# Optimization experiments

Measured on AMD Instinct MI355X. Metric: run time of the kernel, lower is better.

## Reference

```python
import jax, jax.numpy as jnp
from jax import lax
import numpy as np

NUM_HEAD = 12
EPS = 1e-5            # torch LayerNorm default
NEG_INF = 1.0e12      # self.inf_value in the source
LEAKY_SLOPE = 0.01    # torch LeakyReLU default
MASK_FIRST = True     # maskedAtten=True applies only to block 0


def _layer_norm(x, s, b):
    m = jnp.mean(x, axis=-1, keepdims=True)
    v = jnp.var(x, axis=-1, keepdims=True)
    return (x - m) / jnp.sqrt(v + EPS) * s + b


def _forward(x, conv_w, conv_b, pos, ln0_s, ln0_b, Wq, bq, Wk, bk, Wv, bv,
             Wo, bo, ln1_s, ln1_b, W1, b1, W2, b2, proj_w, proj_b):
    B, C, H, W = x.shape
    E = conv_w.shape[0]
    P = conv_w.shape[-1]
    hd = E // NUM_HEAD

    # patch embed: Conv2d(C, E, P, stride=P)
    h = lax.conv_general_dilated(x, conv_w, (P, P), 'VALID',
                                 dimension_numbers=('NCHW', 'OIHW', 'NCHW'))
    h = h + conv_b[None, :, None, None]
    L = h.shape[2] * h.shape[3]
    h = h.reshape(B, E, L).transpose(0, 2, 1) + pos  # (B, L, E)

    causal = jnp.triu(jnp.ones((L, L), dtype=bool), 1)
    n_layers = Wq.shape[0]
    for i in range(n_layers):
        # --- attention block ---
        xn = _layer_norm(h, ln0_s[i], ln0_b[i])
        q = (xn @ Wq[i] + bq[i]).reshape(B, L, NUM_HEAD, hd).transpose(0, 2, 1, 3)
        k = (xn @ Wk[i] + bk[i]).reshape(B, L, NUM_HEAD, hd).transpose(0, 2, 1, 3)
        v = (xn @ Wv[i] + bv[i]).reshape(B, L, NUM_HEAD, hd).transpose(0, 2, 1, 3)
        scores = jnp.einsum('bhqd,bhkd->bhqk', q, k) * (hd ** -0.5)
        if i == 0 and MASK_FIRST:
            scores = jnp.where(causal, -NEG_INF, scores)
        a = jax.nn.softmax(scores, axis=-1)
        o = jnp.einsum('bhqk,bhkd->bhqd', a, v)  # (B, NH, L, hd)
        # faithful to torch source: reshape(bs, l, emb) WITHOUT permuting heads back
        o = o.reshape(B, L, E)
        o = o @ Wo[i] + bo[i]
        h = o + h  # residual onto pre-LN input
        # --- MLP block ---
        xr = _layer_norm(h, ln1_s[i], ln1_b[i])
        m = xr @ W1[i] + b1[i]
        m = jnp.where(m >= 0, m, LEAKY_SLOPE * m)
        m = m @ W2[i] + b2[i]
        h = m + xr  # residual onto post-LN (as in source)

    y = h @ proj_w + proj_b               # (B, L, C*P*P)
    y = y.transpose(0, 2, 1).reshape(B, C, H, W)
    return y


def setup_inputs() -> dict:
    key = jax.random.key(0)
    B, C, H, W = 8, 3, 384, 384
    P, E, NL = 16, 768, 8
    FF = 4 * E
    L = (H // P) * (W // P)  # 576
    CPP = C * P * P          # 768
    s = 0.02
    ks = jax.random.split(key, 24)
    f32 = jnp.float32
    inp = {
        'x': jax.random.normal(ks[0], (B, C, H, W), f32),
        'conv_w': jax.random.normal(ks[1], (E, C, P, P), f32) * s,
        'conv_b': jax.random.normal(ks[2], (E,), f32) * s,
        'pos': jax.random.normal(ks[3], (1, L, E), f32),
        'ln0_s': jnp.ones((NL, E), f32),
        'ln0_b': jnp.zeros((NL, E), f32),
        'Wq': jax.random.normal(ks[4], (NL, E, E), f32) * s,
        'bq': jax.random.normal(ks[5], (NL, E), f32) * s,
        'Wk': jax.random.normal(ks[6], (NL, E, E), f32) * s,
        'bk': jax.random.normal(ks[7], (NL, E), f32) * s,
        'Wv': jax.random.normal(ks[8], (NL, E, E), f32) * s,
        'bv': jax.random.normal(ks[9], (NL, E), f32) * s,
        'Wo': jax.random.normal(ks[10], (NL, E, E), f32) * s,
        'bo': jax.random.normal(ks[11], (NL, E), f32) * s,
        'ln1_s': jnp.ones((NL, E), f32),
        'ln1_b': jnp.zeros((NL, E), f32),
        'W1': jax.random.normal(ks[12], (NL, E, FF), f32) * s,
        'b1': jax.random.normal(ks[13], (NL, FF), f32) * s,
        'W2': jax.random.normal(ks[14], (NL, FF, E), f32) * s,
        'b2': jax.random.normal(ks[15], (NL, E), f32) * s,
        'proj_w': jax.random.normal(ks[16], (E, CPP), f32) * s,
        'proj_b': jax.random.normal(ks[17], (CPP,), f32) * s,
    }
    return inp


def reference(x, conv_w, conv_b, pos, ln0_s, ln0_b, Wq, bq, Wk, bk, Wv, bv,
              Wo, bo, ln1_s, ln1_b, W1, b1, W2, b2, proj_w, proj_b):
    return _forward(x, conv_w, conv_b, pos, ln0_s, ln0_b, Wq, bq, Wk, bk,
                    Wv, bv, Wo, bo, ln1_s, ln1_b, W1, b1, W2, b2,
                    proj_w, proj_b)
```

## Files before the change

kernel.cpp:

```cpp
#include <hip/hip_runtime.h>
#include <hip/hip_bf16.h>
#include <stdint.h>

#define NLAYERS 8
#define LSEQ 576
#define EMB 768
#define NHEAD 12
#define HDIM 64
#define FFDIM 3072
#define BLROWS 4608

typedef __attribute__((ext_vector_type(8))) short short8;
typedef __attribute__((ext_vector_type(4))) float floatx4;

__device__ __forceinline__ float b2f(short s) {
    union { float f; uint32_t u; } x; x.u = ((uint32_t)(uint16_t)s) << 16; return x.f;
}
__device__ __forceinline__ short f2b(float f) {
    union { float f; uint32_t u; } x; x.f = f;
    uint32_t r = x.u + 0x7fffu + ((x.u >> 16) & 1u);
    return (short)(r >> 16);
}

#define GLDS16(gp, lp) __builtin_amdgcn_global_load_lds( \
    (const __attribute__((address_space(1))) void*)(gp), \
    (__attribute__((address_space(3))) void*)(lp), 16, 0, 0)

__device__ __forceinline__ void xcd_remap(int& bx, int& by) {
    const int gx = gridDim.x;
    const int n  = gx * gridDim.y;
    const int orig = by * gx + bx;
    const int q = n >> 3, r = n & 7;
    const int xcd = orig & 7;
    const int wgid = (xcd < r ? xcd * (q + 1) : r * (q + 1) + (xcd - r) * q) + (orig >> 3);
    bx = wgid % gx;
    by = wgid / gx;
}

template<int DEPTH, int RES, bool ADD_POS, bool LEAKY, bool OUT_F32>
__global__ __launch_bounds__(256)
void gemm_bt(const short* __restrict__ A, const short* __restrict__ Bt,
             const float* __restrict__ bias, const float* __restrict__ pos,
             const void* __restrict__ res, void* __restrict__ Cout,
             int N, int K)
{
    __shared__ short As[DEPTH * 64 * 64];
    __shared__ short Bs[DEPTH * 128 * 64];
    int bx = blockIdx.x, by = blockIdx.y;
    xcd_remap(bx, by);
    const int t    = threadIdx.x;
    const int lane = t & 63;
    const int w    = t >> 6;
    const int m0   = by * 64;
    const int n0   = bx * 128;
    const int wm   = (w >> 1) * 32;
    const int wn   = (w & 1) * 64;

    floatx4 acc[2][4];
#pragma unroll
    for (int i = 0; i < 2; ++i)
#pragma unroll
        for (int j = 0; j < 4; ++j)
            acc[i][j] = (floatx4){0.f, 0.f, 0.f, 0.f};

    const int srow = t >> 3;
    const int sch  = t & 7;
    const short* Ag = A  + (size_t)m0 * K;
    const short* Bg = Bt + (size_t)n0 * K;
    const int nt = K >> 6;

#define STAGE(buf, k0)                                                              \
    {                                                                               \
        _Pragma("unroll")                                                           \
        for (int i = 0; i < 2; ++i) {                                               \
            int row = srow + i * 32;                                                \
            GLDS16(Ag + (size_t)row * K + (k0) + ((sch ^ (row & 7)) << 3),          \
                   &As[(buf) * 4096 + (size_t)(t + i * 256) * 8]);                  \
        }                                                                           \
        _Pragma("unroll")                                                           \
        for (int i = 0; i < 4; ++i) {                                               \
            int row = srow + i * 32;                                                \
            GLDS16(Bg + (size_t)row * K + (k0) + ((sch ^ (row & 7)) << 3),          \
                   &Bs[(buf) * 8192 + (size_t)(t + i * 256) * 8]);                  \
        }                                                                           \
    }

#define COMPUTE(buf)                                                                \
    {                                                                               \
        _Pragma("unroll")                                                           \
        for (int ks = 0; ks < 2; ++ks) {                                            \
            short8 af[2], bf[4];                                                    \
            _Pragma("unroll")                                                       \
            for (int i = 0; i < 2; ++i) {                                           \
                int row = wm + i * 16 + (lane & 15);                                \
                int ch  = (ks * 4 + (lane >> 4)) ^ (row & 7);                       \
                af[i] = *(const short8*)&As[(buf) * 4096 + row * 64 + ch * 8];      \
            }                                                                       \
            _Pragma("unroll")                                                       \
            for (int j = 0; j < 4; ++j) {                                           \
                int row = wn + j * 16 + (lane & 15);                                \
                int ch  = (ks * 4 + (lane >> 4)) ^ (row & 7);                       \
                bf[j] = *(const short8*)&Bs[(buf) * 8192 + row * 64 + ch * 8];      \
            }                                                                       \
            _Pragma("unroll")                                                       \
            for (int i = 0; i < 2; ++i)                                             \
                _Pragma("unroll")                                                   \
                for (int j = 0; j < 4; ++j)                                         \
                    acc[i][j] = __builtin_amdgcn_mfma_f32_16x16x32_bf16(            \
                        af[i], bf[j], acc[i][j], 0, 0, 0);                          \
        }                                                                           \
    }

    if constexpr (DEPTH == 2) {
        STAGE(0, 0);
        __syncthreads();
        int cur = 0;
        for (int k0 = 0; k0 < K; k0 += 64) {
            if (k0 + 64 < K) STAGE(cur ^ 1, k0 + 64);
            COMPUTE(cur);
            __syncthreads();
            cur ^= 1;
        }
    } else {
        STAGE(0, 0);
        STAGE(1, 64);
        asm volatile("s_waitcnt vmcnt(6)" ::: "memory");
        __builtin_amdgcn_sched_barrier(0);
        __builtin_amdgcn_s_barrier();
        int cur = 0, stg = 2;
        for (int tt = 0; tt < nt; ++tt) {
            if (tt + 2 < nt) STAGE(stg, (tt + 2) << 6);
            COMPUTE(cur);
            if (tt + 1 < nt) {
                if (tt + 2 < nt) { asm volatile("s_waitcnt vmcnt(6)" ::: "memory"); }
                else             { asm volatile("s_waitcnt vmcnt(0)" ::: "memory"); }
                __builtin_amdgcn_sched_barrier(0);
                __builtin_amdgcn_s_barrier();
                __builtin_amdgcn_sched_barrier(0);
            }
            cur = (cur + 1 == DEPTH) ? 0 : cur + 1;
            stg = (stg + 1 == DEPTH) ? 0 : stg + 1;
        }
    }
#undef STAGE
#undef COMPUTE

    const int colb = n0 + wn + (lane & 15);
    const int rowb = m0 + wm + ((lane >> 4) * 4);
#pragma unroll
    for (int i = 0; i < 2; ++i) {
#pragma unroll
        for (int j = 0; j < 4; ++j) {
            const int col = colb + j * 16;
            const float bv = bias[col];
#pragma unroll
            for (int r = 0; r < 4; ++r) {
                const int row = rowb + i * 16 + r;
                float v = acc[i][j][r] + bv;
                if constexpr (ADD_POS) v += pos[(size_t)(row % LSEQ) * N + col];
                if constexpr (RES == 1) v += ((const float*)res)[(size_t)row * N + col];
                if constexpr (RES == 2) v += b2f(((const short*)res)[(size_t)row * N + col]);
                if constexpr (LEAKY)   v = v >= 0.f ? v : 0.01f * v;
                if constexpr (OUT_F32) ((float*)Cout)[(size_t)row * N + col] = v;
                else                   ((short*)Cout)[(size_t)row * N + col] = f2b(v);
            }
        }
    }
}

__global__ __launch_bounds__(256)
void ln_kernel(const float* __restrict__ h, const float* __restrict__ g,
               const float* __restrict__ bbias, short* __restrict__ outb,
               float* __restrict__ outf)
{
    const int row = blockIdx.x;
    const float* x = h + (size_t)row * EMB;
    const int t = threadIdx.x;
    float v0 = x[t], v1 = x[t + 256], v2 = x[t + 512];
    float s  = v0 + v1 + v2;
    float ss = v0 * v0 + v1 * v1 + v2 * v2;
#pragma unroll
    for (int m = 1; m < 64; m <<= 1) {
        s  += __shfl_xor(s, m, 64);
        ss += __shfl_xor(ss, m, 64);
    }
    __shared__ float red[8];
    if ((t & 63) == 0) { red[t >> 6] = s; red[4 + (t >> 6)] = ss; }
    __syncthreads();
    float S  = red[0] + red[1] + red[2] + red[3];
    float SS = red[4] + red[5] + red[6] + red[7];
    float mean = S * (1.f / 768.f);
    float var  = SS * (1.f / 768.f) - mean * mean;
    float rstd = rsqrtf(var + 1e-5f);
    const size_t base = (size_t)row * EMB;
#pragma unroll
    for (int q = 0; q < 3; ++q) {
        int e = t + q * 256;
        float v = (q == 0 ? v0 : (q == 1 ? v1 : v2));
        float y = (v - mean) * rstd * g[e] + bbias[e];
        outb[base + e] = f2b(y);
        if (outf) outf[base + e] = y;
    }
}

__global__ __launch_bounds__(256)
void repack_kv(const short* __restrict__ qkv, short* __restrict__ kp, short* __restrict__ vt)
{
    const int kt = blockIdx.x, bh = blockIdx.y;
    const int b = bh / 12, h = bh % 12;
    const int t = threadIdx.x;
#pragma unroll
    for (int i = 0; i < 2; ++i) {
        int flat = i * 256 + t;
        int key = flat >> 3, c = flat & 7;
        short8 vK = *(const short8*)(qkv + ((size_t)(b * LSEQ) + kt * 64 + key) * 2304 + 768 + h * 64 + c * 8);
        *(short8*)(kp + ((size_t)bh * LSEQ + kt * 64 + key) * 64 + 8 * (c ^ (key & 7))) = vK;
    }
    __shared__ short tile[64][65];
    const int tx = t & 63, ty = t >> 6;
#pragma unroll
    for (int r = 0; r < 16; ++r) {
        int k = ty * 16 + r;
        tile[k][tx] = qkv[((size_t)(b * LSEQ) + kt * 64 + k) * 2304 + 1536 + h * 64 + tx];
    }
    __syncthreads();
#pragma unroll
    for (int r = 0; r < 16; ++r) {
        int d = ty * 16 + r;
        vt[((size_t)bh * 64 + d) * LSEQ + kt * 64 + (tx ^ ((d & 7) << 3))] = tile[tx][d];
    }
}

__global__ __launch_bounds__(256)
void attn_mfma(const short* __restrict__ qkv, const short* __restrict__ kp,
               const short* __restrict__ vt, short* __restrict__ oout, int causal)
{
    const int qt = blockIdx.x, bh = blockIdx.y;
    const int b = bh / 12, h = bh % 12;
    const int t = threadIdx.x, lane = t & 63, w = t >> 6;

    __shared__ short Ks[64 * 64];
    __shared__ short Vs[64 * 64];
    __shared__ short Plds[4][16][72];

    const int nrow = lane & 15;
    const int kch  = (lane >> 4) * 8;
    const int swz  = (lane & 7) << 3;

    short8 aq[2];
    {
        const short* qrow = qkv + ((size_t)(b * LSEQ) + qt * 64 + w * 16 + nrow) * 2304 + h * 64 + kch;
        aq[0] = *(const short8*)qrow;
        aq[1] = *(const short8*)(qrow + 32);
    }

    float m[4], lsum[4];
    floatx4 oacc[4];
#pragma unroll
    for (int r = 0; r < 4; ++r) { m[r] = -3e38f; lsum[r] = 0.f; }
#pragma unroll
    for (int j = 0; j < 4; ++j) oacc[j] = (floatx4){0.f, 0.f, 0.f, 0.f};

    const int ktend = causal ? qt : 8;
    const short* ksrc = kp + ((size_t)bh * LSEQ) * 64;
    const short* vsrc = vt + ((size_t)bh * 64) * LSEQ;

    for (int kt = 0; kt <= ktend; ++kt) {
        __syncthreads();
        {
            const short* kt_src = ksrc + (size_t)(kt * 64) * 64;
            GLDS16(kt_src + (size_t)t * 8,          &Ks[(size_t)t * 8]);
            GLDS16(kt_src + (size_t)(t + 256) * 8,  &Ks[(size_t)(t + 256) * 8]);
            int f0 = t, f1 = t + 256;
            GLDS16(vsrc + (size_t)(f0 >> 3) * LSEQ + kt * 64 + (f0 & 7) * 8, &Vs[(size_t)f0 * 8]);
            GLDS16(vsrc + (size_t)(f1 >> 3) * LSEQ + kt * 64 + (f1 & 7) * 8, &Vs[(size_t)f1 * 8]);
        }
        __syncthreads();

        floatx4 sc[4];
#pragma unroll
        for (int j = 0; j < 4; ++j) sc[j] = (floatx4){0.f, 0.f, 0.f, 0.f};
#pragma unroll
        for (int s = 0; s < 2; ++s) {
#pragma unroll
            for (int j = 0; j < 4; ++j) {
                short8 bk = *(const short8*)&Ks[(16 * j + nrow) * 64 + ((kch + 32 * s) ^ swz)];
                sc[j] = __builtin_amdgcn_mfma_f32_16x16x32_bf16(aq[s], bk, sc[j], 0, 0, 0);
            }
        }
        float sv[4][4];
#pragma unroll
        for (int j = 0; j < 4; ++j)
#pragma unroll
            for (int r = 0; r < 4; ++r) {
                float v = sc[j][r] * 0.125f;
                if (causal && kt == qt) {
                    int key = kt * 64 + 16 * j + nrow;
                    int qr  = qt * 64 + w * 16 + (lane >> 4) * 4 + r;
                    if (key > qr) v = -1e12f;
                }
                sv[j][r] = v;
            }
#pragma unroll
        for (int r = 0; r < 4; ++r) {
            float tm = fmaxf(fmaxf(sv[0][r], sv[1][r]), fmaxf(sv[2][r], sv[3][r]));
            tm = fmaxf(tm, __shfl_xor(tm, 1, 64));
            tm = fmaxf(tm, __shfl_xor(tm, 2, 64));
            tm = fmaxf(tm, __shfl_xor(tm, 4, 64));
            tm = fmaxf(tm, __shfl_xor(tm, 8, 64));
            float nm = fmaxf(m[r], tm);
            float c  = __expf(m[r] - nm);
            m[r] = nm;
            float ps = 0.f;
#pragma unroll
            for (int j = 0; j < 4; ++j) {
                float p = __expf(sv[j][r] - nm);
                sv[j][r] = p;
                ps += p;
            }
            lsum[r] = lsum[r] * c + ps;
#pragma unroll
            for (int j = 0; j < 4; ++j) oacc[j][r] *= c;
        }
#pragma unroll
        for (int j = 0; j < 4; ++j)
#pragma unroll
            for (int r = 0; r < 4; ++r)
                Plds[w][(lane >> 4) * 4 + r][16 * j + nrow] = f2b(sv[j][r]);
        short8 ap[2];
#pragma unroll
        for (int s = 0; s < 2; ++s)
            ap[s] = *(const short8*)&Plds[w][nrow][kch + 32 * s];
#pragma unroll
        for (int s = 0; s < 2; ++s) {
#pragma unroll
            for (int j = 0; j < 4; ++j) {
                short8 bv = *(const short8*)&Vs[(16 * j + nrow) * 64 + ((kch + 32 * s) ^ swz)];
                oacc[j] = __builtin_amdgcn_mfma_f32_16x16x32_bf16(ap[s], bv, oacc[j], 0, 0, 0);
            }
        }
    }

    float inv[4];
#pragma unroll
    for (int r = 0; r < 4; ++r) {
        float L = lsum[r];
        L += __shfl_xor(L, 1, 64);
        L += __shfl_xor(L, 2, 64);
        L += __shfl_xor(L, 4, 64);
        L += __shfl_xor(L, 8, 64);
        inv[r] = 1.f / L;
    }
#pragma unroll
    for (int j = 0; j < 4; ++j)
#pragma unroll
        for (int r = 0; r < 4; ++r) {
            size_t lq = (size_t)qt * 64 + w * 16 + (lane >> 4) * 4 + r;
            oout[((size_t)bh * LSEQ + lq) * 64 + 16 * j + nrow] = f2b(oacc[j][r] * inv[r]);
        }
}

__global__ void transpose_f2b(const float* __restrict__ in, short* __restrict__ out,
                              int R, int C, long long ibs, long long obs)
{
    __shared__ float tile[32][33];
    const int b = blockIdx.z;
    const float* inb = in + (long long)b * ibs;
    short* outb = out + (long long)b * obs;
    const int r0 = blockIdx.y * 32, c0 = blockIdx.x * 32;
    const int tx = threadIdx.x, ty = threadIdx.y;
#pragma unroll
    for (int i = 0; i < 32; i += 8) tile[ty + i][tx] = inb[(size_t)(r0 + ty + i) * C + c0 + tx];
    __syncthreads();
#pragma unroll
    for (int i = 0; i < 32; i += 8) outb[(size_t)(c0 + ty + i) * R + r0 + tx] = f2b(tile[tx][ty + i]);
}

__global__ void transpose_f2f(const float* __restrict__ in, float* __restrict__ out,
                              int R, int C, long long ibs, long long obs)
{
    __shared__ float tile[32][33];
    const int b = blockIdx.z;
    const float* inb = in + (long long)b * ibs;
    float* outb = out + (long long)b * obs;
    const int r0 = blockIdx.y * 32, c0 = blockIdx.x * 32;
    const int tx = threadIdx.x, ty = threadIdx.y;
#pragma unroll
    for (int i = 0; i < 32; i += 8) tile[ty + i][tx] = inb[(size_t)(r0 + ty + i) * C + c0 + tx];
    __syncthreads();
#pragma unroll
    for (int i = 0; i < 32; i += 8) outb[(size_t)(c0 + ty + i) * R + r0 + tx] = tile[tx][ty + i];
}

__global__ void concat_qkv_bias(const float* __restrict__ bq, const float* __restrict__ bk,
                                const float* __restrict__ bv, float* __restrict__ out)
{
    int i = blockIdx.x * 256 + threadIdx.x;
    int layer = i / 2304, j = i % 2304;
    float v;
    if (j < 768)       v = bq[layer * 768 + j];
    else if (j < 1536) v = bk[layer * 768 + j - 768];
    else               v = bv[layer * 768 + j - 1536];
    out[i] = v;
}

__global__ void im2col_kernel(const float* __restrict__ x, short* __restrict__ xcol)
{
    const size_t idx = (size_t)blockIdx.x * 256 + threadIdx.x;
    const int k = (int)(idx % 768);
    const size_t m = idx / 768;
    const int c  = k >> 8;
    const int ky = (k >> 4) & 15;
    const int kx = k & 15;
    const int b  = (int)(m / 576);
    const int l  = (int)(m % 576);
    const int ph = l / 24, pw = l % 24;
    xcol[idx] = f2b(x[((size_t)(b * 3 + c) * 384 + ph * 16 + ky) * 384 + pw * 16 + kx]);
}

__global__ void cast_f32_b16(const float* __restrict__ in, short* __restrict__ out, int n)
{
    int i = blockIdx.x * 256 + threadIdx.x;
    if (i < n) out[i] = f2b(in[i]);
}

extern "C" void kernel_launch(void* const* d_in, const int* in_sizes, int n_in,
                              void* d_out, int out_size, void* d_ws, size_t ws_size,
                              hipStream_t stream)
{
    const float* x      = (const float*)d_in[0];
    const float* conv_w = (const float*)d_in[1];
    const float* conv_b = (const float*)d_in[2];
    const float* pos    = (const float*)d_in[3];
    const float* ln0_s  = (const float*)d_in[4];
    const float* ln0_b  = (const float*)d_in[5];
    const float* Wq     = (const float*)d_in[6];
    const float* bq     = (const float*)d_in[7];
    const float* Wk     = (const float*)d_in[8];
    const float* bk     = (const float*)d_in[9];
    const float* Wv     = (const float*)d_in[10];
    const float* bv     = (const float*)d_in[11];
    const float* Wo     = (const float*)d_in[12];
    const float* bo     = (const float*)d_in[13];
    const float* ln1_s  = (const float*)d_in[14];
    const float* ln1_b  = (const float*)d_in[15];
    const float* W1     = (const float*)d_in[16];
    const float* b1     = (const float*)d_in[17];
    const float* W2     = (const float*)d_in[18];
    const float* b2     = (const float*)d_in[19];
    const float* proj_w = (const float*)d_in[20];
    const float* proj_b = (const float*)d_in[21];

    char* ws = (char*)d_ws;
    short* qkvT  = (short*)(ws);
    short* woT   = (short*)(ws + 28311552);
    short* w1T   = (short*)(ws + 37748736);
    short* w2T   = (short*)(ws + 75497472);
    short* projT = (short*)(ws + 113246208);
    float* qkvb  = (float*)(ws + 114425856);
    short* tmpA  = (short*)(ws + 114499584);
    float* h     = (float*)(ws + 142811136);
    short* xn    = (short*)(ws + 156966912);
    short* xrb   = (short*)(ws + 164044800);
    short* qkv   = (short*)(ws + 185278464);
    short* o     = (short*)(ws + 206512128);
    short* convB = (short*)(ws + 213590016);

    short* kp = tmpA;
    short* vt = tmpA + 3538944;

    dim3 tb(32, 8);
    transpose_f2b<<<dim3(24, 24, 8), tb, 0, stream>>>(Wq, qkvT,           768, 768, 589824, 1769472);
    transpose_f2b<<<dim3(24, 24, 8), tb, 0, stream>>>(Wk, qkvT + 589824,  768, 768, 589824, 1769472);
    transpose_f2b<<<dim3(24, 24, 8), tb, 0, stream>>>(Wv, qkvT + 1179648, 768, 768, 589824, 1769472);
    transpose_f2b<<<dim3(24, 24, 8), tb, 0, stream>>>(Wo, woT,            768, 768, 589824, 589824);
    transpose_f2b<<<dim3(96, 24, 8), tb, 0, stream>>>(W1, w1T,            768, 3072, 2359296, 2359296);
    transpose_f2b<<<dim3(24, 96, 8), tb, 0, stream>>>(W2, w2T,            3072, 768, 2359296, 2359296);
    transpose_f2b<<<dim3(24, 24, 1), tb, 0, stream>>>(proj_w, projT,      768, 768, 0, 0);
    cast_f32_b16<<<2304, 256, 0, stream>>>(conv_w, convB, 589824);
    concat_qkv_bias<<<72, 256, 0, stream>>>(bq, bk, bv, qkvb);

    im2col_kernel<<<13824, 256, 0, stream>>>(x, tmpA);
    gemm_bt<3, 0, true, false, true><<<dim3(6, 72), 256, 0, stream>>>(
        tmpA, convB, conv_b, pos, nullptr, h, 768, 768);

    for (int i = 0; i < NLAYERS; ++i) {
        ln_kernel<<<4608, 256, 0, stream>>>(h, ln0_s + i * 768, ln0_b + i * 768, xn, nullptr);
        gemm_bt<2, 0, false, false, false><<<dim3(18, 72), 256, 0, stream>>>(
            xn, qkvT + (size_t)i * 1769472, qkvb + i * 2304, nullptr, nullptr, qkv, 2304, 768);
        repack_kv<<<dim3(9, 96), 256, 0, stream>>>(qkv, kp, vt);
        attn_mfma<<<dim3(9, 96), 256, 0, stream>>>(qkv, kp, vt, o, i == 0 ? 1 : 0);
        gemm_bt<3, 1, false, false, true><<<dim3(6, 72), 256, 0, stream>>>(
            o, woT + (size_t)i * 589824, bo + i * 768, nullptr, h, h, 768, 768);
        ln_kernel<<<4608, 256, 0, stream>>>(h, ln1_s + i * 768, ln1_b + i * 768, xrb, nullptr);
        gemm_bt<2, 0, false, true, false><<<dim3(24, 72), 256, 0, stream>>>(
            xrb, w1T + (size_t)i * 2359296, b1 + i * 3072, nullptr, nullptr, tmpA, 3072, 768);
        gemm_bt<3, 2, false, false, true><<<dim3(6, 72), 256, 0, stream>>>(
            tmpA, w2T + (size_t)i * 2359296, b2 + i * 768, nullptr, xrb, h, 768, 3072);
    }

    short* hb = xn;
    float* yf = (float*)tmpA;
    cast_f32_b16<<<13824, 256, 0, stream>>>(h, hb, 4608 * 768);
    gemm_bt<3, 0, false, false, true><<<dim3(6, 72), 256, 0, stream>>>(
        hb, projT, proj_b, nullptr, nullptr, yf, 768, 768);
    transpose_f2f<<<dim3(24, 18, 8), tb, 0, stream>>>(yf, (float*)d_out, 576, 768, 442368, 442368);
}
```

Before: 1.640 ms.

## Fuse K/V repack into QKV GEMM epilogue and bf16 cast into last MLP GEMM

The QKV GEMM epilogue now writes Q to a compact buffer and scatters K and V directly into the swizzled per-head K and transposed V layouts that attention reads. This removes the separate repack_kv kernel and the round trip of the full QKV tensor through memory. The final layer's second MLP GEMM also writes a bf16 copy of its output, which drops the separate cast kernel before the output projection. The cost is scattered 2-byte stores in the QKV epilogue, which are poorly coalesced, especially for the transposed V writes.

```diff
diff --git a/kernel.cpp b/kernel.cpp
--- a/kernel.cpp
+++ b/kernel.cpp
@@ -37,11 +37,12 @@
     by = wgid / gx;
 }
 
-template<int DEPTH, int RES, bool ADD_POS, bool LEAKY, bool OUT_F32>
+template<int DEPTH, int RES, bool ADD_POS, bool LEAKY, int OUTM, bool QKV>
 __global__ __launch_bounds__(256)
 void gemm_bt(const short* __restrict__ A, const short* __restrict__ Bt,
              const float* __restrict__ bias, const float* __restrict__ pos,
              const void* __restrict__ res, void* __restrict__ Cout,
+             short* __restrict__ aux_kp, short* __restrict__ aux_vt,
              int N, int K)
 {
     __shared__ short As[DEPTH * 64 * 64];
@@ -161,8 +162,28 @@
                 if constexpr (RES == 1) v += ((const float*)res)[(size_t)row * N + col];
                 if constexpr (RES == 2) v += b2f(((const short*)res)[(size_t)row * N + col]);
                 if constexpr (LEAKY)   v = v >= 0.f ? v : 0.01f * v;
-                if constexpr (OUT_F32) ((float*)Cout)[(size_t)row * N + col] = v;
-                else                   ((short*)Cout)[(size_t)row * N + col] = f2b(v);
+                if constexpr (QKV) {
+                    const int b = row / LSEQ, l = row % LSEQ;
+                    const short sv16 = f2b(v);
+                    if (col < 768) {
+                        ((short*)Cout)[(size_t)row * 768 + col] = sv16;
+                    } else if (col < 1536) {
+                        const int d = col - 768, hh = d >> 6, dd = d & 63;
+                        const size_t bh = (size_t)b * 12 + hh;
+                        aux_kp[(bh * LSEQ + l) * 64 + (dd & 7) + (((dd >> 3) ^ (l & 7)) << 3)] = sv16;
+                    } else {
+                        const int d = col - 1536, hh = d >> 6, dd = d & 63;
+                        const size_t bh = (size_t)b * 12 + hh;
+                        aux_vt[(bh * 64 + dd) * LSEQ + (l & ~63) + ((l & 63) ^ ((dd & 7) << 3))] = sv16;
+                    }
+                } else if constexpr (OUTM == 1) {
+                    ((float*)Cout)[(size_t)row * N + col] = v;
+                } else if constexpr (OUTM == 2) {
+                    ((float*)Cout)[(size_t)row * N + col] = v;
+                    aux_kp[(size_t)row * N + col] = f2b(v);
+                } else {
+                    ((short*)Cout)[(size_t)row * N + col] = f2b(v);
+                }
             }
         }
     }
@@ -170,8 +191,7 @@
 
 __global__ __launch_bounds__(256)
 void ln_kernel(const float* __restrict__ h, const float* __restrict__ g,
-               const float* __restrict__ bbias, short* __restrict__ outb,
-               float* __restrict__ outf)
+               const float* __restrict__ bbias, short* __restrict__ outb)
 {
     const int row = blockIdx.x;
     const float* x = h + (size_t)row * EMB;
@@ -199,40 +219,11 @@
         float v = (q == 0 ? v0 : (q == 1 ? v1 : v2));
         float y = (v - mean) * rstd * g[e] + bbias[e];
         outb[base + e] = f2b(y);
-        if (outf) outf[base + e] = y;
     }
 }
 
 __global__ __launch_bounds__(256)
-void repack_kv(const short* __restrict__ qkv, short* __restrict__ kp, short* __restrict__ vt)
-{
-    const int kt = blockIdx.x, bh = blockIdx.y;
-    const int b = bh / 12, h = bh % 12;
-    const int t = threadIdx.x;
-#pragma unroll
-    for (int i = 0; i < 2; ++i) {
-        int flat = i * 256 + t;
-        int key = flat >> 3, c = flat & 7;
-        short8 vK = *(const short8*)(qkv + ((size_t)(b * LSEQ) + kt * 64 + key) * 2304 + 768 + h * 64 + c * 8);
-        *(short8*)(kp + ((size_t)bh * LSEQ + kt * 64 + key) * 64 + 8 * (c ^ (key & 7))) = vK;
-    }
-    __shared__ short tile[64][65];
-    const int tx = t & 63, ty = t >> 6;
-#pragma unroll
-    for (int r = 0; r < 16; ++r) {
-        int k = ty * 16 + r;
-        tile[k][tx] = qkv[((size_t)(b * LSEQ) + kt * 64 + k) * 2304 + 1536 + h * 64 + tx];
-    }
-    __syncthreads();
-#pragma unroll
-    for (int r = 0; r < 16; ++r) {
-        int d = ty * 16 + r;
-        vt[((size_t)bh * 64 + d) * LSEQ + kt * 64 + (tx ^ ((d & 7) << 3))] = tile[tx][d];
-    }
-}
-
-__global__ __launch_bounds__(256)
-void attn_mfma(const short* __restrict__ qkv, const short* __restrict__ kp,
+void attn_mfma(const short* __restrict__ qbuf, const short* __restrict__ kp,
                const short* __restrict__ vt, short* __restrict__ oout, int causal)
 {
     const int qt = blockIdx.x, bh = blockIdx.y;
@@ -249,7 +240,7 @@
 
     short8 aq[2];
     {
-        const short* qrow = qkv + ((size_t)(b * LSEQ) + qt * 64 + w * 16 + nrow) * 2304 + h * 64 + kch;
+        const short* qrow = qbuf + ((size_t)(b * LSEQ) + qt * 64 + w * 16 + nrow) * 768 + h * 64 + kch;
         aq[0] = *(const short8*)qrow;
         aq[1] = *(const short8*)(qrow + 32);
     }
@@ -462,7 +453,7 @@
     float* h     = (float*)(ws + 142811136);
     short* xn    = (short*)(ws + 156966912);
     short* xrb   = (short*)(ws + 164044800);
-    short* qkv   = (short*)(ws + 185278464);
+    short* qbuf  = (short*)(ws + 185278464);
     short* o     = (short*)(ws + 206512128);
     short* convB = (short*)(ws + 213590016);
 
@@ -481,28 +472,31 @@
     concat_qkv_bias<<<72, 256, 0, stream>>>(bq, bk, bv, qkvb);
 
     im2col_kernel<<<13824, 256, 0, stream>>>(x, tmpA);
-    gemm_bt<3, 0, true, false, true><<<dim3(6, 72), 256, 0, stream>>>(
-        tmpA, convB, conv_b, pos, nullptr, h, 768, 768);
+    gemm_bt<3, 0, true, false, 1, false><<<dim3(6, 72), 256, 0, stream>>>(
+        tmpA, convB, conv_b, pos, nullptr, h, nullptr, nullptr, 768, 768);
 
     for (int i = 0; i < NLAYERS; ++i) {
-        ln_kernel<<<4608, 256, 0, stream>>>(h, ln0_s + i * 768, ln0_b + i * 768, xn, nullptr);
-        gemm_bt<2, 0, false, false, false><<<dim3(18, 72), 256, 0, stream>>>(
-            xn, qkvT + (size_t)i * 1769472, qkvb + i * 2304, nullptr, nullptr, qkv, 2304, 768);
-        repack_kv<<<dim3(9, 96), 256, 0, stream>>>(qkv, kp, vt);
-        attn_mfma<<<dim3(9, 96), 256, 0, stream>>>(qkv, kp, vt, o, i == 0 ? 1 : 0);
-        gemm_bt<3, 1, false, false, true><<<dim3(6, 72), 256, 0, stream>>>(
-            o, woT + (size_t)i * 589824, bo + i * 768, nullptr, h, h, 768, 768);
-        ln_kernel<<<4608, 256, 0, stream>>>(h, ln1_s + i * 768, ln1_b + i * 768, xrb, nullptr);
-        gemm_bt<2, 0, false, true, false><<<dim3(24, 72), 256, 0, stream>>>(
-            xrb, w1T + (size_t)i * 2359296, b1 + i * 3072, nullptr, nullptr, tmpA, 3072, 768);
-        gemm_bt<3, 2, false, false, true><<<dim3(6, 72), 256, 0, stream>>>(
-            tmpA, w2T + (size_t)i * 2359296, b2 + i * 768, nullptr, xrb, h, 768, 3072);
+        ln_kernel<<<4608, 256, 0, stream>>>(h, ln0_s + i * 768, ln0_b + i * 768, xn);
+        gemm_bt<2, 0, false, false, 0, true><<<dim3(18, 72), 256, 0, stream>>>(
+            xn, qkvT + (size_t)i * 1769472, qkvb + i * 2304, nullptr, nullptr, qbuf, kp, vt, 2304, 768);
+        attn_mfma<<<dim3(9, 96), 256, 0, stream>>>(qbuf, kp, vt, o, i == 0 ? 1 : 0);
+        gemm_bt<3, 1, false, false, 1, false><<<dim3(6, 72), 256, 0, stream>>>(
+            o, woT + (size_t)i * 589824, bo + i * 768, nullptr, h, h, nullptr, nullptr, 768, 768);
+        ln_kernel<<<4608, 256, 0, stream>>>(h, ln1_s + i * 768, ln1_b + i * 768, xrb);
+        gemm_bt<2, 0, false, true, 0, false><<<dim3(24, 72), 256, 0, stream>>>(
+            xrb, w1T + (size_t)i * 2359296, b1 + i * 3072, nullptr, nullptr, tmpA, nullptr, nullptr, 3072, 768);
+        if (i < NLAYERS - 1) {
+            gemm_bt<3, 2, false, false, 1, false><<<dim3(6, 72), 256, 0, stream>>>(
+                tmpA, w2T + (size_t)i * 2359296, b2 + i * 768, nullptr, xrb, h, nullptr, nullptr, 768, 3072);
+        } else {
+            gemm_bt<3, 2, false, false, 2, false><<<dim3(6, 72), 256, 0, stream>>>(
+                tmpA, w2T + (size_t)i * 2359296, b2 + i * 768, nullptr, xrb, h, xn, nullptr, 768, 3072);
+        }
     }
 
     short* hb = xn;
     float* yf = (float*)tmpA;
-    cast_f32_b16<<<13824, 256, 0, stream>>>(h, hb, 4608 * 768);
-    gemm_bt<3, 0, false, false, true><<<dim3(6, 72), 256, 0, stream>>>(
-        hb, projT, proj_b, nullptr, nullptr, yf, 768, 768);
+    gemm_bt<3, 0, false, false, 1, false><<<dim3(6, 72), 256, 0, stream>>>(
+        hb, projT, proj_b, nullptr, nullptr, yf, nullptr, nullptr, 768, 768);
     transpose_f2f<<<dim3(24, 18, 8), tb, 0, stream>>>(yf, (float*)d_out, 576, 768, 442368, 442368);
 }
```

Measured after the change: 1.620 ms. No clear change (-1.2%).
